# Kernel tuning notes

Measured on AMD Instinct MI355X. Metric: run time of the kernel, lower is better.

## Reference

```python
import jax, jax.numpy as jnp
import numpy as np


def setup_inputs() -> dict:
    key = jax.random.key(0)
    kq, kk, kv = jax.random.split(key, 3)
    B, d, N = 8, 768, 6144
    q = jax.random.normal(kq, (B, d, N), dtype=jnp.float32)
    k = jax.random.normal(kk, (B, d, N), dtype=jnp.float32)
    v = jax.random.normal(kv, (B, d, N), dtype=jnp.float32)
    return {"q": q, "k": k, "v": v, "head_dim": 32, "kernel_size": 3}


def reference(q, k, v, head_dim, kernel_size):
    B, d, N = q.shape
    h = d // head_dim          # number of heads
    g = N // kernel_size       # number of local windows
    scale = head_dim ** (-0.5)
    # [B, d, N] -> [B, h, head_dim, ks, g] -> attention layout
    qr = q.reshape(B, h, head_dim, kernel_size, g).transpose(0, 1, 4, 3, 2)  # [B,h,g,ks,hd]
    kr = k.reshape(B, h, head_dim, kernel_size, g).transpose(0, 1, 4, 2, 3)  # [B,h,g,hd,ks]
    vr = v.reshape(B, h, head_dim, kernel_size, g).transpose(0, 1, 4, 3, 2)  # [B,h,g,ks,hd]
    attn = jnp.einsum('bhgkd,bhgdj->bhgkj', qr, kr) * scale                   # [B,h,g,ks,ks]
    attn = jax.nn.softmax(attn, axis=-1)
    x = jnp.einsum('bhgkj,bhgjd->bhgkd', attn, vr)                            # [B,h,g,ks,hd]
    # transpose(1,2) then reshape(B, N, d): [B,g,h,ks,hd] -> [B,N,d]
    return x.transpose(0, 2, 1, 3, 4).reshape(B, N, d)
```

## Files before the change

### kernel.cpp

```cpp
#include <hip/hip_runtime.h>

constexpr int CB = 8;
constexpr int CD = 768;
constexpr int CN = 6144;
constexpr int HD = 32;
constexpr int KS = 3;
constexpr int CH = CD / HD;
constexpr int CG = CN / KS;

__global__ __launch_bounds__(256) void dilate_attn_kernel(
    const float* __restrict__ q, const float* __restrict__ k,
    const float* __restrict__ v, float* __restrict__ out) {
  const int tid  = blockIdx.x * 256 + threadIdx.x;
  const int lane = threadIdx.x & 63;
  const int wav  = tid >> 6;
  const int half = lane >> 5;
  const int wl   = lane & 31;
  const int gg   = (wav & 63) * 32 + wl;
  const int bh   = wav >> 6;
  const int hh   = bh % CH;
  const int b    = bh / CH;

  const size_t rowbase = ((size_t)b * CD + (size_t)(hh * HD + half * 16)) * (size_t)CN
                       + (size_t)gg;
  const float* qb = q + rowbase;
  const float* kb = k + rowbase;
  const float* vb = v + rowbase;

  float s00 = 0.f, s01 = 0.f, s02 = 0.f;
  float s10 = 0.f, s11 = 0.f, s12 = 0.f;
  float s20 = 0.f, s21 = 0.f, s22 = 0.f;
  #pragma unroll 8
  for (int d = 0; d < 16; ++d) {
    const float* qp = qb + (size_t)d * CN;
    const float* kp = kb + (size_t)d * CN;
    const float q0 = qp[0], q1 = qp[CG], q2 = qp[2 * CG];
    const float k0 = kp[0], k1 = kp[CG], k2 = kp[2 * CG];
    s00 = fmaf(q0, k0, s00); s01 = fmaf(q0, k1, s01); s02 = fmaf(q0, k2, s02);
    s10 = fmaf(q1, k0, s10); s11 = fmaf(q1, k1, s11); s12 = fmaf(q1, k2, s12);
    s20 = fmaf(q2, k0, s20); s21 = fmaf(q2, k1, s21); s22 = fmaf(q2, k2, s22);
  }

  s00 += __shfl_xor(s00, 32); s01 += __shfl_xor(s01, 32); s02 += __shfl_xor(s02, 32);
  s10 += __shfl_xor(s10, 32); s11 += __shfl_xor(s11, 32); s12 += __shfl_xor(s12, 32);
  s20 += __shfl_xor(s20, 32); s21 += __shfl_xor(s21, 32); s22 += __shfl_xor(s22, 32);

  const float scale = 0.17677669529663687f;
  s00 *= scale; s01 *= scale; s02 *= scale;
  s10 *= scale; s11 *= scale; s12 *= scale;
  s20 *= scale; s21 *= scale; s22 *= scale;

  const float m0 = fmaxf(fmaxf(s00, s01), s02);
  const float m1 = fmaxf(fmaxf(s10, s11), s12);
  const float m2 = fmaxf(fmaxf(s20, s21), s22);
  const float e00 = __expf(s00 - m0), e01 = __expf(s01 - m0), e02 = __expf(s02 - m0);
  const float e10 = __expf(s10 - m1), e11 = __expf(s11 - m1), e12 = __expf(s12 - m1);
  const float e20 = __expf(s20 - m2), e21 = __expf(s21 - m2), e22 = __expf(s22 - m2);
  const float r0 = 1.f / (e00 + e01 + e02);
  const float r1 = 1.f / (e10 + e11 + e12);
  const float r2 = 1.f / (e20 + e21 + e22);
  const float p00 = e00 * r0, p01 = e01 * r0, p02 = e02 * r0;
  const float p10 = e10 * r1, p11 = e11 * r1, p12 = e12 * r1;
  const float p20 = e20 * r2, p21 = e21 * r2, p22 = e22 * r2;

  float o0[16], o1[16], o2[16];
  #pragma unroll
  for (int d = 0; d < 16; ++d) {
    const float* vp = vb + (size_t)d * CN;
    const float v0 = vp[0], v1 = vp[CG], v2 = vp[2 * CG];
    o0[d] = fmaf(p00, v0, fmaf(p01, v1, p02 * v2));
    o1[d] = fmaf(p10, v0, fmaf(p11, v1, p12 * v2));
    o2[d] = fmaf(p20, v0, fmaf(p21, v1, p22 * v2));
  }

  float* ob = out + ((size_t)b * CG + (size_t)gg) * (size_t)(CH * KS * HD)
                  + (size_t)hh * (KS * HD) + (size_t)half * 16;
  #pragma unroll
  for (int c = 0; c < 4; ++c)
    *reinterpret_cast<float4*>(ob + 0 * HD + c * 4) =
        make_float4(o0[c * 4], o0[c * 4 + 1], o0[c * 4 + 2], o0[c * 4 + 3]);
  #pragma unroll
  for (int c = 0; c < 4; ++c)
    *reinterpret_cast<float4*>(ob + 1 * HD + c * 4) =
        make_float4(o1[c * 4], o1[c * 4 + 1], o1[c * 4 + 2], o1[c * 4 + 3]);
  #pragma unroll
  for (int c = 0; c < 4; ++c)
    *reinterpret_cast<float4*>(ob + 2 * HD + c * 4) =
        make_float4(o2[c * 4], o2[c * 4 + 1], o2[c * 4 + 2], o2[c * 4 + 3]);
}

extern "C" void kernel_launch(void* const* d_in, const int* in_sizes, int n_in,
                              void* d_out, int out_size, void* d_ws, size_t ws_size,
                              hipStream_t stream) {
  const float* q = (const float*)d_in[0];
  const float* k = (const float*)d_in[1];
  const float* v = (const float*)d_in[2];
  float* out = (float*)d_out;

  const int total = CB * CH * CG * 2;
  const int blocks = total / 256;
  dilate_attn_kernel<<<blocks, 256, 0, stream>>>(q, k, v, out);
}
```

Baseline: 129.1 us.

## Split head dim across four lane slices and prefetch V before reduction

Each group's 32-dim head is now split across four 16-lane slices of a wave instead of two halves, so each thread handles 8 dims and twice as many threads are launched. V loads are issued before the shuffle reduction and softmax so their latency overlaps that math. Launch bounds now request 8 blocks per CU to keep register use low. The cost is an extra shuffle stage, and global reads now cover only 16 contiguous floats (64 bytes) per row segment, which coalesces less well.

Result: slower. 176.9 us (+37.1%).

```diff
diff --git a/kernel.cpp b/kernel.cpp
--- a/kernel.cpp
+++ b/kernel.cpp
@@ -8,20 +8,20 @@
 constexpr int CH = CD / HD;
 constexpr int CG = CN / KS;
 
-__global__ __launch_bounds__(256) void dilate_attn_kernel(
+__global__ __launch_bounds__(256, 8) void dilate_attn_kernel(
     const float* __restrict__ q, const float* __restrict__ k,
     const float* __restrict__ v, float* __restrict__ out) {
-  const int tid  = blockIdx.x * 256 + threadIdx.x;
-  const int lane = threadIdx.x & 63;
-  const int wav  = tid >> 6;
-  const int half = lane >> 5;
-  const int wl   = lane & 31;
-  const int gg   = (wav & 63) * 32 + wl;
-  const int bh   = wav >> 6;
-  const int hh   = bh % CH;
-  const int b    = bh / CH;
+  const int tid   = blockIdx.x * 256 + threadIdx.x;
+  const int lane  = threadIdx.x & 63;
+  const int wav   = tid >> 6;
+  const int slice = lane >> 4;
+  const int wl    = lane & 15;
+  const int gg    = (wav & 127) * 16 + wl;
+  const int bh    = wav >> 7;
+  const int hh    = bh % CH;
+  const int b     = bh / CH;
 
-  const size_t rowbase = ((size_t)b * CD + (size_t)(hh * HD + half * 16)) * (size_t)CN
+  const size_t rowbase = ((size_t)b * CD + (size_t)(hh * HD + slice * 8)) * (size_t)CN
                        + (size_t)gg;
   const float* qb = q + rowbase;
   const float* kb = k + rowbase;
@@ -30,8 +30,8 @@
   float s00 = 0.f, s01 = 0.f, s02 = 0.f;
   float s10 = 0.f, s11 = 0.f, s12 = 0.f;
   float s20 = 0.f, s21 = 0.f, s22 = 0.f;
-  #pragma unroll 8
-  for (int d = 0; d < 16; ++d) {
+  #pragma unroll
+  for (int d = 0; d < 8; ++d) {
     const float* qp = qb + (size_t)d * CN;
     const float* kp = kb + (size_t)d * CN;
     const float q0 = qp[0], q1 = qp[CG], q2 = qp[2 * CG];
@@ -41,6 +41,16 @@
     s20 = fmaf(q2, k0, s20); s21 = fmaf(q2, k1, s21); s22 = fmaf(q2, k2, s22);
   }
 
+  float v0v[8], v1v[8], v2v[8];
+  #pragma unroll
+  for (int d = 0; d < 8; ++d) {
+    const float* vp = vb + (size_t)d * CN;
+    v0v[d] = vp[0]; v1v[d] = vp[CG]; v2v[d] = vp[2 * CG];
+  }
+
+  s00 += __shfl_xor(s00, 16); s01 += __shfl_xor(s01, 16); s02 += __shfl_xor(s02, 16);
+  s10 += __shfl_xor(s10, 16); s11 += __shfl_xor(s11, 16); s12 += __shfl_xor(s12, 16);
+  s20 += __shfl_xor(s20, 16); s21 += __shfl_xor(s21, 16); s22 += __shfl_xor(s22, 16);
   s00 += __shfl_xor(s00, 32); s01 += __shfl_xor(s01, 32); s02 += __shfl_xor(s02, 32);
   s10 += __shfl_xor(s10, 32); s11 += __shfl_xor(s11, 32); s12 += __shfl_xor(s12, 32);
   s20 += __shfl_xor(s20, 32); s21 += __shfl_xor(s21, 32); s22 += __shfl_xor(s22, 32);
@@ -63,30 +73,27 @@
   const float p10 = e10 * r1, p11 = e11 * r1, p12 = e12 * r1;
   const float p20 = e20 * r2, p21 = e21 * r2, p22 = e22 * r2;
 
-  float o0[16], o1[16], o2[16];
+  float* ob = out + ((size_t)b * CG + (size_t)gg) * (size_t)(CH * KS * HD)
+                  + (size_t)hh * (KS * HD) + (size_t)slice * 8;
+
+  float o[8];
   #pragma unroll
-  for (int d = 0; d < 16; ++d) {
-    const float* vp = vb + (size_t)d * CN;
-    const float v0 = vp[0], v1 = vp[CG], v2 = vp[2 * CG];
-    o0[d] = fmaf(p00, v0, fmaf(p01, v1, p02 * v2));
-    o1[d] = fmaf(p10, v0, fmaf(p11, v1, p12 * v2));
-    o2[d] = fmaf(p20, v0, fmaf(p21, v1, p22 * v2));
-  }
+  for (int d = 0; d < 8; ++d)
+    o[d] = fmaf(p00, v0v[d], fmaf(p01, v1v[d], p02 * v2v[d]));
+  *reinterpret_cast<float4*>(ob + 0 * HD + 0) = make_float4(o[0], o[1], o[2], o[3]);
+  *reinterpret_cast<float4*>(ob + 0 * HD + 4) = make_float4(o[4], o[5], o[6], o[7]);
 
-  float* ob = out + ((size_t)b * CG + (size_t)gg) * (size_t)(CH * KS * HD)
-                  + (size_t)hh * (KS * HD) + (size_t)half * 16;
   #pragma unroll
-  for (int c = 0; c < 4; ++c)
-    *reinterpret_cast<float4*>(ob + 0 * HD + c * 4) =
-        make_float4(o0[c * 4], o0[c * 4 + 1], o0[c * 4 + 2], o0[c * 4 + 3]);
+  for (int d = 0; d < 8; ++d)
+    o[d] = fmaf(p10, v0v[d], fmaf(p11, v1v[d], p12 * v2v[d]));
+  *reinterpret_cast<float4*>(ob + 1 * HD + 0) = make_float4(o[0], o[1], o[2], o[3]);
+  *reinterpret_cast<float4*>(ob + 1 * HD + 4) = make_float4(o[4], o[5], o[6], o[7]);
+
   #pragma unroll
-  for (int c = 0; c < 4; ++c)
-    *reinterpret_cast<float4*>(ob + 1 * HD + c * 4) =
-        make_float4(o1[c * 4], o1[c * 4 + 1], o1[c * 4 + 2], o1[c * 4 + 3]);
-  #pragma unroll
-  for (int c = 0; c < 4; ++c)
-    *reinterpret_cast<float4*>(ob + 2 * HD + c * 4) =
-        make_float4(o2[c * 4], o2[c * 4 + 1], o2[c * 4 + 2], o2[c * 4 + 3]);
+  for (int d = 0; d < 8; ++d)
+    o[d] = fmaf(p20, v0v[d], fmaf(p21, v1v[d], p22 * v2v[d]));
+  *reinterpret_cast<float4*>(ob + 2 * HD + 0) = make_float4(o[0], o[1], o[2], o[3]);
+  *reinterpret_cast<float4*>(ob + 2 * HD + 4) = make_float4(o[4], o[5], o[6], o[7]);
 }
 
 extern "C" void kernel_launch(void* const* d_in, const int* in_sizes, int n_in,
@@ -97,7 +104,7 @@
   const float* v = (const float*)d_in[2];
   float* out = (float*)d_out;
 
-  const int total = CB * CH * CG * 2;
+  const int total = CB * CH * CG * 4;
   const int blocks = total / 256;
   dilate_attn_kernel<<<blocks, 256, 0, stream>>>(q, k, v, out);
 }
```
